# Kernel optimization log

Measured on AMD Instinct MI355X. Metric: run time of the kernel, lower is better.

The kernel has to match this reference:

```python
import jax, jax.numpy as jnp
import numpy as np

B, N, M = 8, 8192, 1024
C1, C2 = 256, 512
C_IN, C_MID, C_OUT = 768, 256, 256  # mlp = [768, 256, 256]
EPS_BN = 1e-5
EPS_W = 1e-8


def setup_inputs() -> dict:
    key = jax.random.key(0)
    ks = jax.random.split(key, 10)
    inp = {
        "unknown": jax.random.uniform(ks[0], (B, N, 3), dtype=jnp.float32),
        "known": jax.random.uniform(ks[1], (B, M, 3), dtype=jnp.float32),
        "unknow_feats": jax.random.normal(ks[2], (B, C1, N), dtype=jnp.float32),
        "known_feats": jax.random.normal(ks[3], (B, C2, M), dtype=jnp.float32),
        # conv1d (kernel=1) weights, bias-free (followed by BN), per create_convblock1d
        "W1": jax.random.normal(ks[4], (C_MID, C_IN), dtype=jnp.float32) * (1.0 / np.sqrt(C_IN)),
        "g1": jnp.ones((C_MID,), jnp.float32),
        "b1": jnp.zeros((C_MID,), jnp.float32),
        "W2": jax.random.normal(ks[5], (C_OUT, C_MID), dtype=jnp.float32) * (1.0 / np.sqrt(C_MID)),
        "g2": jnp.ones((C_OUT,), jnp.float32),
        "b2": jnp.zeros((C_OUT,), jnp.float32),
    }
    return inp


def _three_interpolation(unknown, known, known_feats):
    # squared pairwise distances (B, N, M), as in pointnet2 three_nn CUDA kernel
    d2 = jnp.sum((unknown[:, :, None, :] - known[:, None, :, :]) ** 2, axis=-1)
    neg_d, idx = jax.lax.top_k(-d2, 3)            # (B, N, 3)
    dist = -neg_d
    w = 1.0 / (dist + EPS_W)
    w = w / jnp.sum(w, axis=-1, keepdims=True)    # (B, N, 3)
    gathered = jax.vmap(lambda f, i: f[:, i])(known_feats, idx)  # (B, C2, N, 3)
    return jnp.einsum("bcnk,bnk->bcn", gathered, w)              # (B, C2, N)


def _conv_bn_relu(x, W, g, b):
    # 1x1 conv1d (no bias) + BatchNorm1d (training-mode stats) + ReLU
    y = jnp.einsum("oc,bcn->bon", W, x)
    mean = jnp.mean(y, axis=(0, 2), keepdims=True)
    var = jnp.var(y, axis=(0, 2), keepdims=True)
    y = (y - mean) * jax.lax.rsqrt(var + EPS_BN)
    y = y * g[None, :, None] + b[None, :, None]
    return jax.nn.relu(y)


def reference(unknown, known, unknow_feats, known_feats, W1, g1, b1, W2, g2, b2):
    interp = _three_interpolation(unknown, known, known_feats)   # (B, C2, N)
    new_features = jnp.concatenate([unknow_feats, interp], axis=1)  # (B, C1+C2, N)
    h = _conv_bn_relu(new_features, W1, g1, b1)
    out = _conv_bn_relu(h, W2, g2, b2)
    return out  # (B, C_OUT, N)
```

## Files before the change

### kernel.cpp

```cpp
#include <hip/hip_runtime.h>

#define B_    8
#define N_    8192
#define M_    1024
#define C1_   256
#define C2_   512
#define CIN_  768
#define CMID_ 256
#define COUT_ 256

typedef __attribute__((ext_vector_type(8))) __bf16 bf16x8;
typedef __attribute__((ext_vector_type(4))) float f32x4;
typedef __attribute__((ext_vector_type(4))) unsigned short u16x4;
typedef __attribute__((ext_vector_type(8))) unsigned short u16x8;

__device__ __forceinline__ unsigned short f2bf(float f) {
  union { float f; unsigned u; } v; v.f = f;
  unsigned r = v.u + 0x7FFFu + ((v.u >> 16) & 1u);
  return (unsigned short)(r >> 16);
}
__device__ __forceinline__ float bf2f(unsigned short h) {
  union { unsigned u; float f; } v; v.u = ((unsigned)h) << 16; return v.f;
}


__global__ void k_zero(float* p, int n) {
  int i = blockIdx.x * 256 + threadIdx.x;
  if (i < n) p[i] = 0.f;
}

__global__ void k_cast(const float* __restrict__ in, unsigned short* __restrict__ out, int n) {
  int i = blockIdx.x * 256 + threadIdx.x;
  if (i < n) out[i] = f2bf(in[i]);
}

__global__ void k_tr_kf(const float* __restrict__ in, float* __restrict__ out) {
  __shared__ float t[32][33];
  int b = blockIdx.z;
  int c0 = blockIdx.x * 32, m0 = blockIdx.y * 32;
  int tx = threadIdx.x, ty = threadIdx.y;
  const float* ip = in + ((size_t)b * C2_ + c0) * M_ + m0;
#pragma unroll
  for (int i = 0; i < 32; i += 8) t[ty + i][tx] = ip[(size_t)(ty + i) * M_ + tx];
  __syncthreads();
  float* op = out + ((size_t)b * M_ + m0) * C2_ + c0;
#pragma unroll
  for (int i = 0; i < 32; i += 8) op[(size_t)(ty + i) * C2_ + tx] = t[tx][ty + i];
}

__global__ void k_tr_uf(const float* __restrict__ in, unsigned short* __restrict__ out) {
  __shared__ float t[32][33];
  int b = blockIdx.z;
  int c0 = blockIdx.x * 32, n0 = blockIdx.y * 32;
  int tx = threadIdx.x, ty = threadIdx.y;
  const float* ip = in + ((size_t)b * C1_ + c0) * N_ + n0;
#pragma unroll
  for (int i = 0; i < 32; i += 8) t[ty + i][tx] = ip[(size_t)(ty + i) * N_ + tx];
  __syncthreads();
  unsigned short* op = out + ((size_t)b * N_ + n0) * CIN_ + c0;
#pragma unroll
  for (int i = 0; i < 32; i += 8) op[(size_t)(ty + i) * CIN_ + tx] = f2bf(t[tx][ty + i]);
}


__device__ __forceinline__ void ins3(float db, int ib, float& d0, int& i0,
                                     float& d1, int& i1, float& d2, int& i2) {
  if (db < d2 || (db == d2 && ib < i2)) {
    if (db < d1 || (db == d1 && ib < i1)) {
      d2 = d1; i2 = i1;
      if (db < d0 || (db == d0 && ib < i0)) { d1 = d0; i1 = i0; d0 = db; i0 = ib; }
      else                                  { d1 = db; i1 = ib; }
    } else { d2 = db; i2 = ib; }
  }
}

__global__ __launch_bounds__(256) void k_three_nn(const float* __restrict__ unknown,
                                                  const float* __restrict__ known,
                                                  int* __restrict__ idx, float* __restrict__ wgt) {
  __shared__ __align__(16) float kpts[M_][4];
  int b = blockIdx.x >> 8;
  int n0 = (blockIdx.x & 255) << 5;
  for (int i = threadIdx.x; i < M_; i += 256) {
    const float* kp = known + ((size_t)b * M_ + i) * 3;
    kpts[i][0] = kp[0]; kpts[i][1] = kp[1]; kpts[i][2] = kp[2];
  }
  __syncthreads();
  const int l = threadIdx.x & 63;
  const int j = l & 7;
  const int q = ((threadIdx.x >> 6) << 3) + (l >> 3);
  const int n = n0 + q;
  const float* up = unknown + ((size_t)b * N_ + n) * 3;
  float ux = up[0], uy = up[1], uz = up[2];
  float d0 = 1e30f, d1 = 1e30f, d2v = 1e30f;
  int i0 = 0, i1 = 0, i2 = 0;
  for (int t = 0; t < 128; ++t) {
    int i = t * 8 + j;
    f32x4 p = *(const f32x4*)kpts[i];
    float dx = __fsub_rn(ux, p[0]);
    float dy = __fsub_rn(uy, p[1]);
    float dz = __fsub_rn(uz, p[2]);
    float d = __fadd_rn(__fadd_rn(__fmul_rn(dx, dx), __fmul_rn(dy, dy)), __fmul_rn(dz, dz));
    if (d < d2v) {
      if (d < d1) {
        if (d < d0) { d2v = d1; i2 = i1; d1 = d0; i1 = i0; d0 = d; i0 = i; }
        else        { d2v = d1; i2 = i1; d1 = d;  i1 = i; }
      } else        { d2v = d;  i2 = i; }
    }
  }
#pragma unroll
  for (int m = 1; m <= 4; m <<= 1) {
    float e0 = __shfl_xor(d0, m), e1 = __shfl_xor(d1, m), e2 = __shfl_xor(d2v, m);
    int   f0 = __shfl_xor(i0, m), f1 = __shfl_xor(i1, m), f2 = __shfl_xor(i2, m);
    ins3(e0, f0, d0, i0, d1, i1, d2v, i2);
    ins3(e1, f1, d0, i0, d1, i1, d2v, i2);
    ins3(e2, f2, d0, i0, d1, i1, d2v, i2);
  }
  if (j == 0) {
    float w0 = 1.f / (d0 + 1e-8f), w1 = 1.f / (d1 + 1e-8f), w2 = 1.f / (d2v + 1e-8f);
    float s = w0 + w1 + w2;
    size_t base = ((size_t)b * N_ + n) * 3;
    idx[base] = i0; idx[base + 1] = i1; idx[base + 2] = i2;
    wgt[base] = w0 / s; wgt[base + 1] = w1 / s; wgt[base + 2] = w2 / s;
  }
}

__global__ __launch_bounds__(256) void k_interp(const float* __restrict__ kft, const int* __restrict__ idx,
                                                const float* __restrict__ wgt, unsigned short* __restrict__ xt) {
  int pb = blockIdx.x * 8 + (threadIdx.x >> 5);
  int lane = threadIdx.x & 31;
  int b = pb >> 13;
  size_t t3 = (size_t)pb * 3;
  int i0 = idx[t3], i1 = idx[t3 + 1], i2 = idx[t3 + 2];
  float w0 = wgt[t3], w1 = wgt[t3 + 1], w2 = wgt[t3 + 2];
  const f32x4* f0 = (const f32x4*)(kft + ((size_t)b * M_ + i0) * C2_);
  const f32x4* f1 = (const f32x4*)(kft + ((size_t)b * M_ + i1) * C2_);
  const f32x4* f2 = (const f32x4*)(kft + ((size_t)b * M_ + i2) * C2_);
  unsigned short* o = xt + (size_t)pb * CIN_ + C1_;
#pragma unroll
  for (int k = 0; k < 4; ++k) {
    int c4 = lane + 32 * k;
    f32x4 a = f0[c4], bb = f1[c4], cc = f2[c4];
    u16x4 r;
#pragma unroll
    for (int e = 0; e < 4; ++e) r[e] = f2bf(w0 * a[e] + w1 * bb[e] + w2 * cc[e]);
    *(u16x4*)(o + 4 * c4) = r;
  }
}


template <int K, int EPI>
__global__ __launch_bounds__(256) void gemm_bt(const unsigned short* __restrict__ A,
                                               const unsigned short* __restrict__ Bm,
                                               unsigned short* __restrict__ C) {
  __shared__ __align__(16) char lds[32768];
  const int tid = threadIdx.x;
  const int l = tid & 63;
  const int wv = tid >> 6;
  const int wr = wv >> 1, wc = wv & 1;
  const int b = blockIdx.z;
  const int o0 = blockIdx.y * 128;
  const int n0 = blockIdx.x * 128;
  const char* Ab = (const char*)A + (size_t)o0 * (K * 2);
  const char* Bb = (const char*)Bm + ((size_t)b * N_ + n0) * (K * 2);

  f32x4 zero = {0.f, 0.f, 0.f, 0.f};
  f32x4 acc[4][4];
#pragma unroll
  for (int i = 0; i < 4; ++i)
#pragma unroll
    for (int j = 0; j < 4; ++j) acc[i][j] = zero;

  int srow[4], scol[4];
#pragma unroll
  for (int i = 0; i < 4; ++i) { int q = tid + i * 256; srow[i] = q >> 3; scol[i] = (q & 7) * 16; }

  bf16x8 ra[4], rb[4];
#pragma unroll
  for (int i = 0; i < 4; ++i) {
    ra[i] = *(const bf16x8*)(Ab + (size_t)srow[i] * (K * 2) + scol[i]);
    rb[i] = *(const bf16x8*)(Bb + (size_t)srow[i] * (K * 2) + scol[i]);
  }

  const int NK = K / 64;
  for (int kt = 0; kt < NK; ++kt) {
    __syncthreads();
#pragma unroll
    for (int i = 0; i < 4; ++i) {
      int d = srow[i] * 128 + (scol[i] ^ ((srow[i] & 7) << 4));
      *(bf16x8*)(lds + d) = ra[i];
      *(bf16x8*)(lds + 16384 + d) = rb[i];
    }
    __syncthreads();
    if (kt + 1 < NK) {
      const char* Ak = Ab + (size_t)(kt + 1) * 128;
      const char* Bk = Bb + (size_t)(kt + 1) * 128;
#pragma unroll
      for (int i = 0; i < 4; ++i) {
        ra[i] = *(const bf16x8*)(Ak + (size_t)srow[i] * (K * 2) + scol[i]);
        rb[i] = *(const bf16x8*)(Bk + (size_t)srow[i] * (K * 2) + scol[i]);
      }
    }
#pragma unroll
    for (int kk = 0; kk < 2; ++kk) {
      bf16x8 af[4], bfr[4];
#pragma unroll
      for (int mi = 0; mi < 4; ++mi) {
        int row = wr * 64 + mi * 16 + (l & 15);
        int cb = (kk * 64 + ((l >> 4) * 16)) ^ ((row & 7) << 4);
        af[mi] = *(const bf16x8*)(lds + row * 128 + cb);
      }
#pragma unroll
      for (int ni = 0; ni < 4; ++ni) {
        int row = wc * 64 + ni * 16 + (l & 15);
        int cb = (kk * 64 + ((l >> 4) * 16)) ^ ((row & 7) << 4);
        bfr[ni] = *(const bf16x8*)(lds + 16384 + row * 128 + cb);
      }
#pragma unroll
      for (int mi = 0; mi < 4; ++mi)
#pragma unroll
        for (int ni = 0; ni < 4; ++ni)
          acc[mi][ni] = __builtin_amdgcn_mfma_f32_16x16x32_bf16(af[mi], bfr[ni], acc[mi][ni], 0, 0, 0);
    }
  }

#pragma unroll
  for (int mi = 0; mi < 4; ++mi) {
    int o = o0 + wr * 64 + mi * 16 + ((l >> 4) << 2);
#pragma unroll
    for (int ni = 0; ni < 4; ++ni) {
      int n = n0 + wc * 64 + ni * 16 + (l & 15);
      if (EPI == 0) {
        u16x4 pk;
#pragma unroll
        for (int r = 0; r < 4; ++r) pk[r] = f2bf(acc[mi][ni][r]);
        *(u16x4*)(C + ((size_t)b * N_ + n) * 256 + o) = pk;
      } else {
#pragma unroll
        for (int r = 0; r < 4; ++r)
          C[((size_t)b * 256 + (o + r)) * N_ + n] = f2bf(acc[mi][ni][r]);
      }
    }
  }
}


__global__ void k_stats_pm(const unsigned short* __restrict__ y, float* __restrict__ sum,
                           float* __restrict__ sq) {
  int c = threadIdx.x;
  size_t r0 = (size_t)blockIdx.x * 128;
  float s = 0.f, s2 = 0.f;
  for (int r = 0; r < 128; ++r) {
    float v = bf2f(y[(r0 + r) * 256 + c]);
    s += v; s2 = fmaf(v, v, s2);
  }
  atomicAdd(&sum[c], s); atomicAdd(&sq[c], s2);
}

__global__ void k_stats_cm(const unsigned short* __restrict__ y, float* __restrict__ sum,
                           float* __restrict__ sq) {
  int bo = blockIdx.x;
  int o = bo & 255;
  const unsigned short* p = y + (size_t)bo * N_;
  float s = 0.f, s2 = 0.f;
  for (int i = threadIdx.x; i < N_; i += 256) { float v = bf2f(p[i]); s += v; s2 = fmaf(v, v, s2); }
#pragma unroll
  for (int off = 32; off; off >>= 1) { s += __shfl_down(s, off); s2 += __shfl_down(s2, off); }
  __shared__ float rs[4], rq[4];
  if ((threadIdx.x & 63) == 0) { rs[threadIdx.x >> 6] = s; rq[threadIdx.x >> 6] = s2; }
  __syncthreads();
  if (threadIdx.x == 0) {
    atomicAdd(&sum[o], rs[0] + rs[1] + rs[2] + rs[3]);
    atomicAdd(&sq[o],  rq[0] + rq[1] + rq[2] + rq[3]);
  }
}

__global__ void k_finalize(const float* __restrict__ sum, const float* __restrict__ sq,
                           const float* __restrict__ g, const float* __restrict__ bb,
                           float* __restrict__ scale, float* __restrict__ shift) {
  int c = threadIdx.x;
  const float inv_n = 1.f / 65536.f;
  float mean = sum[c] * inv_n;
  float var = sq[c] * inv_n - mean * mean;
  float rstd = rsqrtf(var + 1e-5f);
  float sc = g[c] * rstd;
  scale[c] = sc;
  shift[c] = bb[c] - mean * sc;
}

__global__ void k_bnrelu_pm(unsigned short* __restrict__ y, const float* __restrict__ scale,
                            const float* __restrict__ shift) {
  __shared__ float sc[256], sh[256];
  sc[threadIdx.x] = scale[threadIdx.x]; sh[threadIdx.x] = shift[threadIdx.x];
  __syncthreads();
  size_t i = ((size_t)blockIdx.x * 256 + threadIdx.x) * 8;
  int c0 = (int)(i & 255);
  u16x8 v = *(const u16x8*)(y + i);
  u16x8 r;
#pragma unroll
  for (int k = 0; k < 8; ++k) {
    float f = bf2f(v[k]) * sc[c0 + k] + sh[c0 + k];
    r[k] = f2bf(fmaxf(f, 0.f));
  }
  *(u16x8*)(y + i) = r;
}

__global__ void k_bnrelu_out(const unsigned short* __restrict__ y, const float* __restrict__ scale,
                             const float* __restrict__ shift, float* __restrict__ out) {
  size_t i = ((size_t)blockIdx.x * 256 + threadIdx.x) * 4;
  int c = (int)((i >> 13) & 255);
  float sc = scale[c], sh = shift[c];
  u16x4 v = *(const u16x4*)(y + i);
  f32x4 o;
#pragma unroll
  for (int k = 0; k < 4; ++k) o[k] = fmaxf(bf2f(v[k]) * sc + sh, 0.f);
  *(f32x4*)(out + i) = o;
}


extern "C" void kernel_launch(void* const* d_in, const int* in_sizes, int n_in,
                              void* d_out, int out_size, void* d_ws, size_t ws_size,
                              hipStream_t stream) {
  const float* unknown = (const float*)d_in[0];
  const float* known   = (const float*)d_in[1];
  const float* uf      = (const float*)d_in[2];
  const float* kf      = (const float*)d_in[3];
  const float* W1      = (const float*)d_in[4];
  const float* g1      = (const float*)d_in[5];
  const float* b1      = (const float*)d_in[6];
  const float* W2      = (const float*)d_in[7];
  const float* g2      = (const float*)d_in[8];
  const float* b2      = (const float*)d_in[9];
  float* out = (float*)d_out;

  char* ws = (char*)d_ws;
  unsigned short* xt  = (unsigned short*)(ws);
  unsigned short* y1  = (unsigned short*)(ws + 100663296);
  unsigned short* y2  = (unsigned short*)(ws + 134217728);
  float*          kft = (float*)(ws + 167772160);
  unsigned short* w1b = (unsigned short*)(ws + 184549376);
  unsigned short* w2b = (unsigned short*)(ws + 184942592);
  int*            idx = (int*)(ws + 185073664);
  float*          wgt = (float*)(ws + 185860096);
  float*          st  = (float*)(ws + 186646528);
  float *sum1 = st, *sq1 = st + 256, *sum2 = st + 512, *sq2 = st + 768;
  float *sc1 = st + 1024, *sh1 = st + 1280, *sc2 = st + 1536, *sh2 = st + 1792;

  k_zero<<<4, 256, 0, stream>>>(st, 1024);
  k_cast<<<768, 256, 0, stream>>>(W1, w1b, CMID_ * CIN_);
  k_cast<<<256, 256, 0, stream>>>(W2, w2b, COUT_ * CMID_);
  k_tr_kf<<<dim3(16, 32, B_), dim3(32, 8), 0, stream>>>(kf, kft);
  k_tr_uf<<<dim3(8, 256, B_), dim3(32, 8), 0, stream>>>(uf, xt);
  k_three_nn<<<B_ * 256, 256, 0, stream>>>(unknown, known, idx, wgt);
  k_interp<<<B_ * N_ / 8, 256, 0, stream>>>(kft, idx, wgt, xt);
  gemm_bt<CIN_, 0><<<dim3(64, 2, B_), 256, 0, stream>>>(w1b, xt, y1);
  k_stats_pm<<<512, 256, 0, stream>>>(y1, sum1, sq1);
  k_finalize<<<1, 256, 0, stream>>>(sum1, sq1, g1, b1, sc1, sh1);
  k_bnrelu_pm<<<8192, 256, 0, stream>>>(y1, sc1, sh1);
  gemm_bt<CMID_, 1><<<dim3(64, 2, B_), 256, 0, stream>>>(w2b, y1, y2);
  k_stats_cm<<<2048, 256, 0, stream>>>(y2, sum2, sq2);
  k_finalize<<<1, 256, 0, stream>>>(sum2, sq2, g2, b2, sc2, sh2);
  k_bnrelu_out<<<16384, 256, 0, stream>>>(y2, sc2, sh2, out);
}
```

Baseline: 230.4 us.

## Fuse BN statistics and BN+ReLU into GEMMs, use direct global-to-LDS loads

Batch-norm sum and sum-of-squares are now reduced in the GEMM epilogue with shuffles and atomics, which removes the separate stats kernels. The first BN+ReLU is applied while the second GEMM loads its B operand, so the in-place normalisation pass over y1 is gone. Operand tiles are now copied with global_load_lds straight into LDS, which drops the XOR swizzle and the register staging. Risks: stats are computed from fp32 accumulators rather than from bf16-rounded values, the unswizzled LDS reads may cause bank conflicts, and there is less prefetch overlap since loads are no longer issued for the next tile ahead of time.

```diff
diff --git a/kernel.cpp b/kernel.cpp
--- a/kernel.cpp
+++ b/kernel.cpp
@@ -21,6 +21,11 @@
 }
 __device__ __forceinline__ float bf2f(unsigned short h) {
   union { unsigned u; float f; } v; v.u = ((unsigned)h) << 16; return v.f;
+}
+
+__device__ __forceinline__ void gload16(const void* g, void* l) {
+  __builtin_amdgcn_global_load_lds((const __attribute__((address_space(1))) unsigned int*)g,
+                                   (__attribute__((address_space(3))) unsigned int*)l, 16, 0, 0);
 }
 
 
@@ -148,11 +153,15 @@
 }
 
 
-template <int K, int EPI>
+template <int K, int EPI, bool BN>
 __global__ __launch_bounds__(256) void gemm_bt(const unsigned short* __restrict__ A,
                                                const unsigned short* __restrict__ Bm,
-                                               unsigned short* __restrict__ C) {
+                                               unsigned short* __restrict__ C,
+                                               float* __restrict__ sum, float* __restrict__ sq,
+                                               const float* __restrict__ scale,
+                                               const float* __restrict__ shift) {
   __shared__ __align__(16) char lds[32768];
+  __shared__ float lsc[256], lsh[256];
   const int tid = threadIdx.x;
   const int l = tid & 63;
   const int wv = tid >> 6;
@@ -163,6 +172,8 @@
   const char* Ab = (const char*)A + (size_t)o0 * (K * 2);
   const char* Bb = (const char*)Bm + ((size_t)b * N_ + n0) * (K * 2);
 
+  if (BN) { lsc[tid] = scale[tid]; lsh[tid] = shift[tid]; }
+
   f32x4 zero = {0.f, 0.f, 0.f, 0.f};
   f32x4 acc[4][4];
 #pragma unroll
@@ -170,15 +181,17 @@
 #pragma unroll
     for (int j = 0; j < 4; ++j) acc[i][j] = zero;
 
+  const int grow = wv * 32 + (l >> 3);
+  const int gcol = (l & 7) * 16;
   int srow[4], scol[4];
 #pragma unroll
   for (int i = 0; i < 4; ++i) { int q = tid + i * 256; srow[i] = q >> 3; scol[i] = (q & 7) * 16; }
 
-  bf16x8 ra[4], rb[4];
-#pragma unroll
-  for (int i = 0; i < 4; ++i) {
-    ra[i] = *(const bf16x8*)(Ab + (size_t)srow[i] * (K * 2) + scol[i]);
-    rb[i] = *(const bf16x8*)(Bb + (size_t)srow[i] * (K * 2) + scol[i]);
+  bf16x8 rb[4];
+  if (BN) {
+#pragma unroll
+    for (int i = 0; i < 4; ++i)
+      rb[i] = *(const bf16x8*)(Bb + (size_t)srow[i] * (K * 2) + scol[i]);
   }
 
   const int NK = K / 64;
@@ -186,19 +199,31 @@
     __syncthreads();
 #pragma unroll
     for (int i = 0; i < 4; ++i) {
-      int d = srow[i] * 128 + (scol[i] ^ ((srow[i] & 7) << 4));
-      *(bf16x8*)(lds + d) = ra[i];
-      *(bf16x8*)(lds + 16384 + d) = rb[i];
+      int r = grow + i * 8;
+      gload16(Ab + (size_t)r * (K * 2) + kt * 128 + gcol, lds + wv * 4096 + i * 1024);
+      if (!BN)
+        gload16(Bb + (size_t)r * (K * 2) + kt * 128 + gcol, lds + 16384 + wv * 4096 + i * 1024);
+    }
+    if (BN) {
+#pragma unroll
+      for (int i = 0; i < 4; ++i) {
+        u16x8 v = *(u16x8*)&rb[i];
+        u16x8 r;
+        int c0 = kt * 64 + (scol[i] >> 1);
+#pragma unroll
+        for (int e = 0; e < 8; ++e) {
+          float f = bf2f(v[e]) * lsc[c0 + e] + lsh[c0 + e];
+          r[e] = f2bf(fmaxf(f, 0.f));
+        }
+        *(u16x8*)(lds + 16384 + srow[i] * 128 + scol[i]) = r;
+      }
     }
     __syncthreads();
-    if (kt + 1 < NK) {
-      const char* Ak = Ab + (size_t)(kt + 1) * 128;
+    if (BN && kt + 1 < NK) {
       const char* Bk = Bb + (size_t)(kt + 1) * 128;
 #pragma unroll
-      for (int i = 0; i < 4; ++i) {
-        ra[i] = *(const bf16x8*)(Ak + (size_t)srow[i] * (K * 2) + scol[i]);
+      for (int i = 0; i < 4; ++i)
         rb[i] = *(const bf16x8*)(Bk + (size_t)srow[i] * (K * 2) + scol[i]);
-      }
     }
 #pragma unroll
     for (int kk = 0; kk < 2; ++kk) {
@@ -206,14 +231,12 @@
 #pragma unroll
       for (int mi = 0; mi < 4; ++mi) {
         int row = wr * 64 + mi * 16 + (l & 15);
-        int cb = (kk * 64 + ((l >> 4) * 16)) ^ ((row & 7) << 4);
-        af[mi] = *(const bf16x8*)(lds + row * 128 + cb);
+        af[mi] = *(const bf16x8*)(lds + row * 128 + kk * 64 + (l >> 4) * 16);
       }
 #pragma unroll
       for (int ni = 0; ni < 4; ++ni) {
         int row = wc * 64 + ni * 16 + (l & 15);
-        int cb = (kk * 64 + ((l >> 4) * 16)) ^ ((row & 7) << 4);
-        bfr[ni] = *(const bf16x8*)(lds + 16384 + row * 128 + cb);
+        bfr[ni] = *(const bf16x8*)(lds + 16384 + row * 128 + kk * 64 + (l >> 4) * 16);
       }
 #pragma unroll
       for (int mi = 0; mi < 4; ++mi)
@@ -241,38 +264,26 @@
       }
     }
   }
-}
-
-
-__global__ void k_stats_pm(const unsigned short* __restrict__ y, float* __restrict__ sum,
-                           float* __restrict__ sq) {
-  int c = threadIdx.x;
-  size_t r0 = (size_t)blockIdx.x * 128;
-  float s = 0.f, s2 = 0.f;
-  for (int r = 0; r < 128; ++r) {
-    float v = bf2f(y[(r0 + r) * 256 + c]);
-    s += v; s2 = fmaf(v, v, s2);
-  }
-  atomicAdd(&sum[c], s); atomicAdd(&sq[c], s2);
-}
-
-__global__ void k_stats_cm(const unsigned short* __restrict__ y, float* __restrict__ sum,
-                           float* __restrict__ sq) {
-  int bo = blockIdx.x;
-  int o = bo & 255;
-  const unsigned short* p = y + (size_t)bo * N_;
-  float s = 0.f, s2 = 0.f;
-  for (int i = threadIdx.x; i < N_; i += 256) { float v = bf2f(p[i]); s += v; s2 = fmaf(v, v, s2); }
-#pragma unroll
-  for (int off = 32; off; off >>= 1) { s += __shfl_down(s, off); s2 += __shfl_down(s2, off); }
-  __shared__ float rs[4], rq[4];
-  if ((threadIdx.x & 63) == 0) { rs[threadIdx.x >> 6] = s; rq[threadIdx.x >> 6] = s2; }
-  __syncthreads();
-  if (threadIdx.x == 0) {
-    atomicAdd(&sum[o], rs[0] + rs[1] + rs[2] + rs[3]);
-    atomicAdd(&sq[o],  rq[0] + rq[1] + rq[2] + rq[3]);
-  }
-}
+
+#pragma unroll
+  for (int mi = 0; mi < 4; ++mi) {
+    float s[4] = {0.f, 0.f, 0.f, 0.f}, q[4] = {0.f, 0.f, 0.f, 0.f};
+#pragma unroll
+    for (int ni = 0; ni < 4; ++ni)
+#pragma unroll
+      for (int r = 0; r < 4; ++r) { float v = acc[mi][ni][r]; s[r] += v; q[r] = fmaf(v, v, q[r]); }
+#pragma unroll
+    for (int m = 1; m <= 8; m <<= 1)
+#pragma unroll
+      for (int r = 0; r < 4; ++r) { s[r] += __shfl_xor(s[r], m); q[r] += __shfl_xor(q[r], m); }
+    if ((l & 15) == 0) {
+      int o = o0 + wr * 64 + mi * 16 + ((l >> 4) << 2);
+#pragma unroll
+      for (int r = 0; r < 4; ++r) { atomicAdd(&sum[o + r], s[r]); atomicAdd(&sq[o + r], q[r]); }
+    }
+  }
+}
+
 
 __global__ void k_finalize(const float* __restrict__ sum, const float* __restrict__ sq,
                            const float* __restrict__ g, const float* __restrict__ bb,
@@ -285,23 +296,6 @@
   float sc = g[c] * rstd;
   scale[c] = sc;
   shift[c] = bb[c] - mean * sc;
-}
-
-__global__ void k_bnrelu_pm(unsigned short* __restrict__ y, const float* __restrict__ scale,
-                            const float* __restrict__ shift) {
-  __shared__ float sc[256], sh[256];
-  sc[threadIdx.x] = scale[threadIdx.x]; sh[threadIdx.x] = shift[threadIdx.x];
-  __syncthreads();
-  size_t i = ((size_t)blockIdx.x * 256 + threadIdx.x) * 8;
-  int c0 = (int)(i & 255);
-  u16x8 v = *(const u16x8*)(y + i);
-  u16x8 r;
-#pragma unroll
-  for (int k = 0; k < 8; ++k) {
-    float f = bf2f(v[k]) * sc[c0 + k] + sh[c0 + k];
-    r[k] = f2bf(fmaxf(f, 0.f));
-  }
-  *(u16x8*)(y + i) = r;
 }
 
 __global__ void k_bnrelu_out(const unsigned short* __restrict__ y, const float* __restrict__ scale,
@@ -352,12 +346,9 @@
   k_tr_uf<<<dim3(8, 256, B_), dim3(32, 8), 0, stream>>>(uf, xt);
   k_three_nn<<<B_ * 256, 256, 0, stream>>>(unknown, known, idx, wgt);
   k_interp<<<B_ * N_ / 8, 256, 0, stream>>>(kft, idx, wgt, xt);
-  gemm_bt<CIN_, 0><<<dim3(64, 2, B_), 256, 0, stream>>>(w1b, xt, y1);
-  k_stats_pm<<<512, 256, 0, stream>>>(y1, sum1, sq1);
+  gemm_bt<CIN_, 0, false><<<dim3(64, 2, B_), 256, 0, stream>>>(w1b, xt, y1, sum1, sq1, nullptr, nullptr);
   k_finalize<<<1, 256, 0, stream>>>(sum1, sq1, g1, b1, sc1, sh1);
-  k_bnrelu_pm<<<8192, 256, 0, stream>>>(y1, sc1, sh1);
-  gemm_bt<CMID_, 1><<<dim3(64, 2, B_), 256, 0, stream>>>(w2b, y1, y2);
-  k_stats_cm<<<2048, 256, 0, stream>>>(y2, sum2, sq2);
+  gemm_bt<CMID_, 1, true><<<dim3(64, 2, B_), 256, 0, stream>>>(w2b, y1, y2, sum2, sq2, sc1, sh1);
   k_finalize<<<1, 256, 0, stream>>>(sum2, sq2, g2, b2, sc2, sh2);
   k_bnrelu_out<<<16384, 256, 0, stream>>>(y2, sc2, sh2, out);
 }
```

New measurement: 377.7 us. 1.64x slower.
